# Kernel tuning notes

Measured on AMD Instinct MI355X. Metric: run time of the kernel, lower is better.

The kernel has to match this reference:

```python
import jax, jax.numpy as jnp
import numpy as np

B, S, D, H, E = 4, 1024, 1024, 4096, 8


def setup_inputs() -> dict:
    key = jax.random.key(0)
    ks = jax.random.split(key, 5)
    sd = 1.0 / np.sqrt(D)
    sh = 1.0 / np.sqrt(H)
    x = jax.random.normal(ks[0], (B, S, D), dtype=jnp.float32)
    # stacked expert weights: Linear(D->H), ReLU, Linear(H->D)
    W1 = jax.random.normal(ks[1], (E, D, H), dtype=jnp.float32) * sd
    b1 = jnp.zeros((E, H), dtype=jnp.float32)
    W2 = jax.random.normal(ks[2], (E, H, D), dtype=jnp.float32) * sh
    b2 = jnp.zeros((E, D), dtype=jnp.float32)
    # gate Linear(D->E)
    Wg = jax.random.normal(ks[3], (D, E), dtype=jnp.float32) * sd
    bg = jnp.zeros((E,), dtype=jnp.float32)
    return {"x": x, "W1": W1, "b1": b1, "W2": W2, "b2": b2,
            "Wg": Wg, "bg": bg, "top_k": 2}


def reference(x, W1, b1, W2, b2, Wg, bg, top_k):
    # gating
    gating_scores = jnp.einsum('bsd,de->bse', x, Wg) + bg          # [B,S,E]
    gating_probs = jax.nn.softmax(gating_scores, axis=-1)
    _, top_k_indices = jax.lax.top_k(gating_probs, top_k)          # [B,S,K]
    n_exp = Wg.shape[1]
    # per-token 0/1 mask of selected experts (matches torch sum over k of mask)
    # NOTE: original code multiplies by the binary mask only; top_k_probs are
    # computed but NOT used as combine weights. We reproduce that faithfully.
    sel = jnp.sum(top_k_indices[..., None] == jnp.arange(n_exp), axis=2)  # [B,S,E]
    sel = sel.astype(x.dtype)
    # dense all-experts FFN (as the original does)
    h = jax.nn.relu(jnp.einsum('bsd,edh->bseh', x, W1) + b1)       # [B,S,E,H]
    eo = jnp.einsum('bseh,ehd->bsed', h, W2) + b2                  # [B,S,E,D]
    output = jnp.einsum('bsed,bse->bsd', eo, sel)                  # [B,S,D]
    return (output, gating_scores)
```

## Files before the change

### kernel.cpp

```cpp
#include <hip/hip_runtime.h>
#include <hip/hip_bf16.h>
#include <stdint.h>

#define B_ 4
#define S_ 1024
#define D_ 1024
#define H_ 4096
#define E_ 8
#define T_ (B_*S_)

#define GBM 128
#define BK 64
#define MAXT1 2432
#define MAXT2 1280

typedef __bf16 bf16x8 __attribute__((ext_vector_type(8)));
typedef float f32x4 __attribute__((ext_vector_type(4)));
typedef unsigned short ushort8 __attribute__((ext_vector_type(8)));

__device__ __forceinline__ unsigned short f2bf(float f) {
  union { float f; uint32_t u; } v; v.f = f;
  uint32_t u = v.u;
  u += 0x7fff + ((u >> 16) & 1);
  return (unsigned short)(u >> 16);
}

__device__ __forceinline__ void gl16(const void* g, void* l) {
  __builtin_amdgcn_global_load_lds(
      (const __attribute__((address_space(1))) void*)g,
      (__attribute__((address_space(3))) void*)l,
      16, 0, 0);
}

__global__ __launch_bounds__(256) void conv_x_kernel(
    const float* __restrict__ x, unsigned short* __restrict__ xb) {
  size_t i = ((size_t)blockIdx.x * 256 + threadIdx.x) * 8;
  const float4* s = (const float4*)(x + i);
  float4 v0 = s[0], v1 = s[1];
  ushort8 w;
  w[0]=f2bf(v0.x); w[1]=f2bf(v0.y); w[2]=f2bf(v0.z); w[3]=f2bf(v0.w);
  w[4]=f2bf(v1.x); w[5]=f2bf(v1.y); w[6]=f2bf(v1.z); w[7]=f2bf(v1.w);
  *(ushort8*)(xb + i) = w;
}

__global__ __launch_bounds__(256) void transpose_conv(
    const float* __restrict__ in, unsigned short* __restrict__ outp,
    int R, int C) {
  __shared__ float tile[64][68];
  const int e = blockIdx.z;
  const size_t eoff = (size_t)e * R * C;
  const int r0 = blockIdx.y * 64, c0 = blockIdx.x * 64;
  const int t = threadIdx.x;
  {
    const int r = t >> 2, cq = (t & 3) * 16;
    const float4* s4 = (const float4*)(in + eoff + (size_t)(r0 + r) * C + (c0 + cq));
#pragma unroll
    for (int i = 0; i < 4; ++i)
      *(float4*)&tile[r][cq + i * 4] = s4[i];
  }
  __syncthreads();
  {
    const int c = t >> 2, r8 = (t & 3) * 16;
    unsigned short* dst = outp + eoff + (size_t)(c0 + c) * R + (r0 + r8);
    ushort8 w0, w1;
#pragma unroll
    for (int j = 0; j < 8; ++j) {
      w0[j] = f2bf(tile[r8 + j][c]);
      w1[j] = f2bf(tile[r8 + 8 + j][c]);
    }
    *(ushort8*)dst = w0;
    *(ushort8*)(dst + 8) = w1;
  }
}

__global__ __launch_bounds__(256) void gating_kernel(
    const float* __restrict__ x, const float* __restrict__ Wg,
    const float* __restrict__ bg, float* __restrict__ scores,
    int* __restrict__ cnt, int* __restrict__ lists) {
  int t = blockIdx.x * 4 + (threadIdx.x >> 6);
  int l = threadIdx.x & 63;
  float acc[E_];
#pragma unroll
  for (int e = 0; e < E_; ++e) acc[e] = 0.f;
  const float* xr = x + (size_t)t * D_;
  for (int k = l; k < D_; k += 64) {
    float xv = xr[k];
    const float4* w = (const float4*)(Wg + (size_t)k * E_);
    float4 w0 = w[0], w1 = w[1];
    acc[0] += xv * w0.x; acc[1] += xv * w0.y; acc[2] += xv * w0.z; acc[3] += xv * w0.w;
    acc[4] += xv * w1.x; acc[5] += xv * w1.y; acc[6] += xv * w1.z; acc[7] += xv * w1.w;
  }
#pragma unroll
  for (int off = 32; off > 0; off >>= 1)
#pragma unroll
    for (int e = 0; e < E_; ++e) acc[e] += __shfl_xor(acc[e], off, 64);
  if (l == 0) {
    float s[E_];
#pragma unroll
    for (int e = 0; e < E_; ++e) {
      s[e] = acc[e] + bg[e];
      scores[(size_t)t * E_ + e] = s[e];
    }
    int i1 = 0; float m1 = -1e30f;
#pragma unroll
    for (int e = 0; e < E_; ++e) if (s[e] > m1) { m1 = s[e]; i1 = e; }
    int i2 = -1; float m2 = -1e30f;
#pragma unroll
    for (int e = 0; e < E_; ++e) if (e != i1 && s[e] > m2) { m2 = s[e]; i2 = e; }
    int p1 = atomicAdd(&cnt[i1], 1); lists[i1 * T_ + p1] = t;
    int p2 = atomicAdd(&cnt[i2], 1); lists[i2 * T_ + p2] = t;
  }
}

__global__ void scan_kernel(const int* __restrict__ cnt, int* __restrict__ off,
                            int* __restrict__ hdr, int* __restrict__ t1tab,
                            int* __restrict__ t2tab) {
  if (threadIdx.x == 0) {
    int o = 0;
    int mtiles[E_];
    for (int e = 0; e < E_; ++e) {
      off[e] = o; o += cnt[e];
      mtiles[e] = (cnt[e] + GBM - 1) / GBM;
    }
    int n1 = 0;
    for (int e = 0; e < E_; ++e)
      for (int nt = 0; nt < H_ / GBM; ++nt)
        for (int mt = 0; mt < mtiles[e]; ++mt)
          t1tab[n1++] = (e << 16) | (mt << 8) | nt;
    int n2 = 0;
    for (int e = 0; e < E_; ++e)
      for (int sp = 0; sp < 2; ++sp)
        for (int nt = 0; nt < D_ / GBM; ++nt)
          for (int mt = 0; mt < mtiles[e]; ++mt)
            t2tab[n2++] = (e << 16) | (mt << 8) | (sp << 6) | nt;
    hdr[0] = n1; hdr[1] = n2;
  }
}

template <int LAYER, int SPLITK>
__global__ __launch_bounds__(256, 3) void ffn_gemm(
    const unsigned short* __restrict__ xb,
    const unsigned short* __restrict__ hbuf,
    const unsigned short* __restrict__ WT,
    const float* __restrict__ bias,
    const int* __restrict__ cnt, const int* __restrict__ off,
    const int* __restrict__ lists,
    const int* __restrict__ tab, const int* __restrict__ hdr,
    unsigned short* __restrict__ hout,
    float* __restrict__ out)
{
  constexpr int K = (LAYER == 1) ? D_ : H_;
  constexpr int N = (LAYER == 1) ? H_ : D_;
  constexpr int KS = K / SPLITK;
  constexpr int NT = KS / BK;

  const int ntask = hdr[LAYER - 1];
  const int b = blockIdx.x;
  if (b >= ntask) return;
  const int q = ntask >> 3, r = ntask & 7;
  const int x = b & 7, ii = b >> 3;
  const int task = (x < r ? x * (q + 1) : r * (q + 1) + (x - r) * q) + ii;

  const int ent = tab[task];
  const int e  = ent >> 16;
  const int m0 = ((ent >> 8) & 0xff) * GBM;
  const int sp = (ent >> 6) & 3;
  const int n0 = (ent & 63) * GBM;
  const int k0 = sp * KS;
  const int count = cnt[e];
  const int oe = off[e];
  const int* lst = lists + e * T_;

  __shared__ unsigned short sA[GBM * BK];
  __shared__ unsigned short sB[GBM * BK];

  const int tid  = threadIdx.x;
  const int lane = tid & 63;
  const int wv   = tid >> 6;
  const int wm   = (wv >> 1) * 64;
  const int wn   = (wv & 1) * 64;

  const int srow   = lane >> 3;
  const int schunk = (lane & 7) * 16;
  const int sgoff  = schunk ^ (srow << 4);

  const char* arow[4];
  const char* brow[4];
#pragma unroll
  for (int i = 0; i < 4; ++i) {
    int rr = i * 32 + wv * 8 + srow;
    int gr = m0 + rr;
    if (LAYER == 1) {
      int tok = (gr < count) ? lst[gr] : lst[m0];
      arow[i] = (const char*)(xb + (size_t)tok * K + k0);
    } else {
      int r2 = (gr < count) ? gr : m0;
      arow[i] = (const char*)(hbuf + (size_t)(oe + r2) * K + k0);
    }
    brow[i] = (const char*)(WT + (size_t)e * N * K + (size_t)(n0 + rr) * K + k0);
  }

  const int lrow = lane & 15;
  const int kg   = lane >> 4;
  const int fswz = (lrow & 7) << 4;

  f32x4 acc[4][4];
#pragma unroll
  for (int i = 0; i < 4; ++i)
#pragma unroll
    for (int j = 0; j < 4; ++j) acc[i][j] = (f32x4){0.f, 0.f, 0.f, 0.f};

#pragma unroll 1
  for (int t = 0; t < NT; ++t) {
    const int kb = t * 128;
#pragma unroll
    for (int i = 0; i < 4; ++i)
      gl16(arow[i] + kb + sgoff, (char*)sA + (i * 32 + wv * 8) * 128);
#pragma unroll
    for (int i = 0; i < 4; ++i)
      gl16(brow[i] + kb + sgoff, (char*)sB + (i * 32 + wv * 8) * 128);
    __syncthreads();
#pragma unroll
    for (int ks = 0; ks < 2; ++ks) {
      bf16x8 af[4], bfm[4];
      const int kbyte = ks * 64 + kg * 16;
#pragma unroll
      for (int i = 0; i < 4; ++i) {
        af[i]  = *(const bf16x8*)((const char*)sA + (wm + i * 16 + lrow) * 128 + (kbyte ^ fswz));
        bfm[i] = *(const bf16x8*)((const char*)sB + (wn + i * 16 + lrow) * 128 + (kbyte ^ fswz));
      }
#pragma unroll
      for (int i = 0; i < 4; ++i)
#pragma unroll
        for (int j = 0; j < 4; ++j)
          acc[i][j] = __builtin_amdgcn_mfma_f32_16x16x32_bf16(af[i], bfm[j], acc[i][j], 0, 0, 0);
    }
    __syncthreads();
  }

  const int rbase = 4 * kg;
#pragma unroll
  for (int i = 0; i < 4; ++i) {
#pragma unroll
    for (int r2 = 0; r2 < 4; ++r2) {
      int row  = wm + i * 16 + rbase + r2;
      int grow = m0 + row;
      if (grow < count) {
#pragma unroll
        for (int j = 0; j < 4; ++j) {
          int col  = wn + j * 16 + lrow;
          int gcol = n0 + col;
          float bv = (SPLITK == 1 || sp == 0) ? bias[(size_t)e * N + gcol] : 0.f;
          float v = acc[i][j][r2] + bv;
          if (LAYER == 1) {
            v = v > 0.f ? v : 0.f;
            hout[(size_t)(oe + grow) * H_ + gcol] = f2bf(v);
          } else {
            int tok = lst[grow];
            atomicAdd(&out[(size_t)tok * D_ + gcol], v);
          }
        }
      }
    }
  }
}

extern "C" void kernel_launch(void* const* d_in, const int* in_sizes, int n_in,
                              void* d_out, int out_size, void* d_ws, size_t ws_size,
                              hipStream_t stream) {
  (void)in_sizes; (void)n_in; (void)out_size; (void)ws_size;
  const float* x  = (const float*)d_in[0];
  const float* W1 = (const float*)d_in[1];
  const float* b1 = (const float*)d_in[2];
  const float* W2 = (const float*)d_in[3];
  const float* b2 = (const float*)d_in[4];
  const float* Wg = (const float*)d_in[5];
  const float* bg = (const float*)d_in[6];

  float* out    = (float*)d_out;
  float* scores = out + (size_t)T_ * D_;

  char* ws = (char*)d_ws;
  int* cnt   = (int*)ws;
  int* off   = (int*)(ws + 32);
  int* hdr   = (int*)(ws + 64);
  int* t1tab = (int*)(ws + 128);
  int* t2tab = (int*)(ws + 10240);
  int* lists = (int*)(ws + 16384);
  unsigned short* xb   = (unsigned short*)(ws + 16384 + 131072);
  unsigned short* hbuf = (unsigned short*)(ws + 16384 + 131072 + 8388608);
  unsigned short* WT   = (unsigned short*)(ws + 16384 + 131072 + 8388608 + 67108864);

  hipMemsetAsync(out, 0, (size_t)T_ * D_ * sizeof(float), stream);
  hipMemsetAsync(cnt, 0, 64, stream);

  conv_x_kernel<<<(T_ * D_) / (256 * 8), 256, 0, stream>>>(x, xb);
  gating_kernel<<<T_ / 4, 256, 0, stream>>>(x, Wg, bg, scores, cnt, lists);
  scan_kernel<<<1, 64, 0, stream>>>(cnt, off, hdr, t1tab, t2tab);

  transpose_conv<<<dim3(H_ / 64, D_ / 64, E_), 256, 0, stream>>>(W1, WT, D_, H_);
  ffn_gemm<1, 1><<<MAXT1, 256, 0, stream>>>(
      xb, hbuf, WT, b1, cnt, off, lists, t1tab, hdr, hbuf, nullptr);

  transpose_conv<<<dim3(D_ / 64, H_ / 64, E_), 256, 0, stream>>>(W2, WT, H_, D_);
  ffn_gemm<2, 2><<<MAXT2, 256, 0, stream>>>(
      xb, hbuf, WT, b2, cnt, off, lists, t2tab, hdr, nullptr, out);
}
```

Baseline: 496.9 us.

## Fuse x bf16 conversion into gating, convert weights before transpose, raise occupancy

The separate x-to-bf16 conversion kernel is folded into the gating kernel, which already reads x. That removes one launch and a second full pass over x. The weight transpose now converts to bf16 before staging in shared memory, which halves the LDS tile size and moves conversion off the strided read path. The GEMM launch bounds ask for 4 blocks per CU instead of 3, which may force register spills.

```diff
diff --git a/kernel.cpp b/kernel.cpp
--- a/kernel.cpp
+++ b/kernel.cpp
@@ -17,6 +17,7 @@
 typedef __bf16 bf16x8 __attribute__((ext_vector_type(8)));
 typedef float f32x4 __attribute__((ext_vector_type(4)));
 typedef unsigned short ushort8 __attribute__((ext_vector_type(8)));
+typedef unsigned short ushort4v __attribute__((ext_vector_type(4)));
 
 __device__ __forceinline__ unsigned short f2bf(float f) {
   union { float f; uint32_t u; } v; v.f = f;
@@ -32,43 +33,37 @@
       16, 0, 0);
 }
 
-__global__ __launch_bounds__(256) void conv_x_kernel(
-    const float* __restrict__ x, unsigned short* __restrict__ xb) {
-  size_t i = ((size_t)blockIdx.x * 256 + threadIdx.x) * 8;
-  const float4* s = (const float4*)(x + i);
-  float4 v0 = s[0], v1 = s[1];
-  ushort8 w;
-  w[0]=f2bf(v0.x); w[1]=f2bf(v0.y); w[2]=f2bf(v0.z); w[3]=f2bf(v0.w);
-  w[4]=f2bf(v1.x); w[5]=f2bf(v1.y); w[6]=f2bf(v1.z); w[7]=f2bf(v1.w);
-  *(ushort8*)(xb + i) = w;
-}
-
 __global__ __launch_bounds__(256) void transpose_conv(
     const float* __restrict__ in, unsigned short* __restrict__ outp,
     int R, int C) {
-  __shared__ float tile[64][68];
+  __shared__ unsigned short tile[64][66];
   const int e = blockIdx.z;
   const size_t eoff = (size_t)e * R * C;
   const int r0 = blockIdx.y * 64, c0 = blockIdx.x * 64;
   const int t = threadIdx.x;
   {
-    const int r = t >> 2, cq = (t & 3) * 16;
-    const float4* s4 = (const float4*)(in + eoff + (size_t)(r0 + r) * C + (c0 + cq));
-#pragma unroll
-    for (int i = 0; i < 4; ++i)
-      *(float4*)&tile[r][cq + i * 4] = s4[i];
+    const int r = t >> 2, cseg = (t & 3) * 16;
+    const float4* s4 = (const float4*)(in + eoff + (size_t)(r0 + r) * C + (c0 + cseg));
+    float4 v0 = s4[0], v1 = s4[1], v2 = s4[2], v3 = s4[3];
+    ushort8 w0, w1;
+    w0[0]=f2bf(v0.x); w0[1]=f2bf(v0.y); w0[2]=f2bf(v0.z); w0[3]=f2bf(v0.w);
+    w0[4]=f2bf(v1.x); w0[5]=f2bf(v1.y); w0[6]=f2bf(v1.z); w0[7]=f2bf(v1.w);
+    w1[0]=f2bf(v2.x); w1[1]=f2bf(v2.y); w1[2]=f2bf(v2.z); w1[3]=f2bf(v2.w);
+    w1[4]=f2bf(v3.x); w1[5]=f2bf(v3.y); w1[6]=f2bf(v3.z); w1[7]=f2bf(v3.w);
+    *(ushort8*)&tile[r][cseg]     = w0;
+    *(ushort8*)&tile[r][cseg + 8] = w1;
   }
   __syncthreads();
   {
-    const int c = t >> 2, r8 = (t & 3) * 16;
-    unsigned short* dst = outp + eoff + (size_t)(c0 + c) * R + (r0 + r8);
+    const int c = t >> 2, rseg = (t & 3) * 16;
     ushort8 w0, w1;
 #pragma unroll
     for (int j = 0; j < 8; ++j) {
-      w0[j] = f2bf(tile[r8 + j][c]);
-      w1[j] = f2bf(tile[r8 + 8 + j][c]);
-    }
-    *(ushort8*)dst = w0;
+      w0[j] = tile[rseg + j][c];
+      w1[j] = tile[rseg + 8 + j][c];
+    }
+    unsigned short* dst = outp + eoff + (size_t)(c0 + c) * R + (r0 + rseg);
+    *(ushort8*)dst       = w0;
     *(ushort8*)(dst + 8) = w1;
   }
 }
@@ -76,6 +71,7 @@
 __global__ __launch_bounds__(256) void gating_kernel(
     const float* __restrict__ x, const float* __restrict__ Wg,
     const float* __restrict__ bg, float* __restrict__ scores,
+    unsigned short* __restrict__ xb,
     int* __restrict__ cnt, int* __restrict__ lists) {
   int t = blockIdx.x * 4 + (threadIdx.x >> 6);
   int l = threadIdx.x & 63;
@@ -83,12 +79,20 @@
 #pragma unroll
   for (int e = 0; e < E_; ++e) acc[e] = 0.f;
   const float* xr = x + (size_t)t * D_;
-  for (int k = l; k < D_; k += 64) {
-    float xv = xr[k];
-    const float4* w = (const float4*)(Wg + (size_t)k * E_);
-    float4 w0 = w[0], w1 = w[1];
-    acc[0] += xv * w0.x; acc[1] += xv * w0.y; acc[2] += xv * w0.z; acc[3] += xv * w0.w;
-    acc[4] += xv * w1.x; acc[5] += xv * w1.y; acc[6] += xv * w1.z; acc[7] += xv * w1.w;
+  unsigned short* xbr = xb + (size_t)t * D_;
+  for (int k4 = l * 4; k4 < D_; k4 += 256) {
+    float4 xv = *(const float4*)(xr + k4);
+    ushort4v wq;
+    wq[0] = f2bf(xv.x); wq[1] = f2bf(xv.y); wq[2] = f2bf(xv.z); wq[3] = f2bf(xv.w);
+    *(ushort4v*)(xbr + k4) = wq;
+#pragma unroll
+    for (int q = 0; q < 4; ++q) {
+      float xs = (q == 0) ? xv.x : (q == 1) ? xv.y : (q == 2) ? xv.z : xv.w;
+      const float4* w = (const float4*)(Wg + (size_t)(k4 + q) * E_);
+      float4 w0 = w[0], w1 = w[1];
+      acc[0] += xs * w0.x; acc[1] += xs * w0.y; acc[2] += xs * w0.z; acc[3] += xs * w0.w;
+      acc[4] += xs * w1.x; acc[5] += xs * w1.y; acc[6] += xs * w1.z; acc[7] += xs * w1.w;
+    }
   }
 #pragma unroll
   for (int off = 32; off > 0; off >>= 1)
@@ -138,7 +142,7 @@
 }
 
 template <int LAYER, int SPLITK>
-__global__ __launch_bounds__(256, 3) void ffn_gemm(
+__global__ __launch_bounds__(256, 4) void ffn_gemm(
     const unsigned short* __restrict__ xb,
     const unsigned short* __restrict__ hbuf,
     const unsigned short* __restrict__ WT,
@@ -294,8 +298,7 @@
   hipMemsetAsync(out, 0, (size_t)T_ * D_ * sizeof(float), stream);
   hipMemsetAsync(cnt, 0, 64, stream);
 
-  conv_x_kernel<<<(T_ * D_) / (256 * 8), 256, 0, stream>>>(x, xb);
-  gating_kernel<<<T_ / 4, 256, 0, stream>>>(x, Wg, bg, scores, cnt, lists);
+  gating_kernel<<<T_ / 4, 256, 0, stream>>>(x, Wg, bg, scores, xb, cnt, lists);
   scan_kernel<<<1, 64, 0, stream>>>(cnt, off, hdr, t1tab, t2tab);
 
   transpose_conv<<<dim3(H_ / 64, D_ / 64, E_), 256, 0, stream>>>(W1, WT, D_, H_);
```

Measured after the change: 492.8 us. No clear change (-0.8%).
